# Kernel tuning notes

Measured on AMD Instinct MI355X. Metric: run time of the kernel, lower is better.

## Reference

```python
import jax, jax.numpy as jnp
import numpy as np

B, T, C = 2, 1024, 1024
H = 16
D = C // H          # 64 head_dim
NHH = 4             # hyper n_heads
NL = 2              # hyper n_layers
RANK = 8
SCALE = 16.0 / RANK # alpha / rank


def _rope(x, cos, sin):
    # x: (B,H,T,D); cos/sin: (1,1,T,D//2)
    xe, xo = x[..., ::2], x[..., 1::2]
    return jnp.stack((xe * cos - xo * sin, xe * sin + xo * cos), axis=-1).reshape(x.shape)


def _mha(x, w_in, b_in, w_out, b_out, mask):
    # torch nn.MultiheadAttention (batch_first) with additive causal mask
    b, t, d = x.shape
    dh = d // NHH
    qkv = x @ w_in.T + b_in
    q, k, v = jnp.split(qkv, 3, axis=-1)
    split = lambda z: z.reshape(b, t, NHH, dh).transpose(0, 2, 1, 3)
    q, k, v = split(q), split(k), split(v)
    s = jnp.einsum('bhqd,bhkd->bhqk', q, k) / jnp.sqrt(jnp.float32(dh)) + mask
    o = jnp.einsum('bhqk,bhkd->bhqd', jax.nn.softmax(s, axis=-1), v)
    o = o.transpose(0, 2, 1, 3).reshape(b, t, d)
    return o @ w_out.T + b_out


def _tiny_head(x_h, in_w, in_b, out_w, out_b, a_w, b_w, mask):
    # x_h: (B,T,D); per-layer params stacked on axis 0 (NL)
    out = x_h
    for l in range(NL):
        out = _mha(out, in_w[l], in_b[l], out_w[l], out_b[l], mask)
    ctx = out.mean(axis=1)                       # (B,D)
    A = (ctx @ a_w.T).reshape(-1, D, RANK)       # (B,D,R)
    Bm = (ctx @ b_w.T).reshape(-1, RANK, D)      # (B,R,D)
    return A, Bm


def reference(x, cos, sin, c_attn_w, c_attn_b, c_proj_w, c_proj_b,
              hyper_in_w, hyper_in_b, hyper_out_w, hyper_out_b, toA_w, toB_w):
    mask = jnp.where(jnp.tril(jnp.ones((T, T), bool)), 0.0, -jnp.inf).astype(x.dtype)
    qkv = x @ c_attn_w.T + c_attn_b
    q, k, v = jnp.split(qkv, 3, axis=-1)
    split = lambda z: z.reshape(B, T, H, D).transpose(0, 2, 1, 3)  # (B,H,T,D)
    q, k, v = split(q), split(k), split(v)
    q = _rope(q, cos, sin)
    k = _rope(k, cos, sin)
    x_heads = split(x)
    # vmap over the 16 main heads; each gets its own TinyHeadTransformer params
    A, Bm = jax.vmap(_tiny_head, in_axes=(1, 0, 0, 0, 0, 0, 0, None))(
        x_heads, hyper_in_w, hyper_in_b, hyper_out_w, hyper_out_b, toA_w, toB_w, mask)
    # A: (H,B,D,R), Bm: (H,B,R,D)
    delta_v = jnp.einsum('bhti,hbir,hbro->bhto', v, A, Bm)
    v = v + SCALE * delta_v
    s = jnp.einsum('bhqd,bhkd->bhqk', q, k) / jnp.sqrt(jnp.float32(D)) + mask
    y = jnp.einsum('bhqk,bhkd->bhqd', jax.nn.softmax(s, axis=-1), v)
    y = y.transpose(0, 2, 1, 3).reshape(B, T, C)
    return y @ c_proj_w.T + c_proj_b


def setup_inputs() -> dict:
    key = jax.random.key(0)
    ks = jax.random.split(key, 8)
    inv_freq = 1.0 / (10000.0 ** (jnp.arange(0, D, 2, dtype=jnp.float32) / D))
    ang = jnp.arange(T, dtype=jnp.float32)[:, None] * inv_freq[None, :]
    cos = jnp.cos(ang)[None, None]  # (1,1,T,D/2)
    sin = jnp.sin(ang)[None, None]
    g = lambda k, shape, sc: jax.random.normal(k, shape, jnp.float32) * sc
    return dict(
        x=g(ks[0], (B, T, C), 1.0),
        cos=cos, sin=sin,
        c_attn_w=g(ks[1], (3 * C, C), 0.02),
        c_attn_b=jnp.zeros((3 * C,), jnp.float32),
        c_proj_w=g(ks[2], (C, C), 0.02),
        c_proj_b=jnp.zeros((C,), jnp.float32),
        hyper_in_w=g(ks[3], (H, NL, 3 * D, D), 0.02),
        hyper_in_b=jnp.zeros((H, NL, 3 * D), jnp.float32),
        hyper_out_w=g(ks[4], (H, NL, D, D), 0.02),
        hyper_out_b=jnp.zeros((H, NL, D), jnp.float32),
        toA_w=g(ks[5], (H, D * RANK, D), 0.02),
        toB_w=g(ks[6], (H, RANK * D, D), 0.02),
    )
```

## Files before the change

### kernel.cpp

```cpp
#include <hip/hip_runtime.h>

typedef unsigned short u16;
typedef short v8s __attribute__((ext_vector_type(8)));
typedef short v4s16 __attribute__((ext_vector_type(4)));
typedef float v4f __attribute__((ext_vector_type(4)));

#if defined(__has_builtin)
#  if __has_builtin(__builtin_amdgcn_exp2f)
#    define EXP2F(x) __builtin_amdgcn_exp2f(x)
#  else
#    define EXP2F(x) exp2f(x)
#  endif
#else
#  define EXP2F(x) exp2f(x)
#endif

__device__ __forceinline__ float bf2f(u16 u){
  union { float f; unsigned int i; } c; c.i = ((unsigned int)u) << 16; return c.f;
}
__device__ __forceinline__ u16 f2bf(float f){
  union { float f; unsigned int i; } c; c.f = f;
  unsigned int r = c.i + 0x7FFFu + ((c.i >> 16) & 1u);
  return (u16)(r >> 16);
}
__device__ __forceinline__ unsigned int cvt_pk_bf16(float lo, float hi){
  unsigned int r;
  asm("v_cvt_pk_bf16_f32 %0, %1, %2" : "=v"(r) : "v"(lo), "v"(hi));
  return r;
}

struct CvtArgs {
  const float* s[13];
  u16* d[13];
  int n[13];
  int bstart[14];
  float* ctxz;
};
__global__ __launch_bounds__(256) void cvt_all(CvtArgs a) {
  if ((int)blockIdx.x >= a.bstart[13]) {
    float4 z = {0.f, 0.f, 0.f, 0.f};
    ((float4*)a.ctxz)[threadIdx.x] = z;
    ((float4*)a.ctxz)[256 + threadIdx.x] = z;
    return;
  }
  int j = 0;
  #pragma unroll
  for (int i = 1; i < 13; i++) if ((int)blockIdx.x >= a.bstart[i]) j = i;
  const int lb = blockIdx.x - a.bstart[j];
  const long base = (long)lb * 1024 + threadIdx.x * 4;
  if (base < a.n[j]) {
    const float4 f = *(const float4*)&a.s[j][base];
    v4s16 o;
    o.x = (short)f2bf(f.x); o.y = (short)f2bf(f.y);
    o.z = (short)f2bf(f.z); o.w = (short)f2bf(f.w);
    *(v4s16*)&a.d[j][base] = o;
  }
}

template<int BM, int BN, int EPI>
__global__ __launch_bounds__(256) void gemm_nt(
    const u16* __restrict__ A, long aBatch, int lda,
    const u16* __restrict__ W, long wBatch,
    const u16* __restrict__ bias, long bBatch,
    void* __restrict__ Cp, long cBatch, int ldc,
    int K,
    const u16* __restrict__ cosb, const u16* __restrict__ sinb,
    u16* __restrict__ q_r, u16* __restrict__ k_r, u16* __restrict__ v_out,
    float* __restrict__ ctxp)
{
  constexpr int BK = 64, LDT = BK + 8;
  constexpr int AC = BM / 32;
  constexpr int BC = BN / 32;
  A    += (long)blockIdx.z * aBatch;
  W    += (long)blockIdx.z * wBatch;
  bias += (long)blockIdx.z * bBatch;
  const int row0 = blockIdx.y * BM, col0 = blockIdx.x * BN;
  __shared__ __align__(16) u16 As[BM * LDT];
  __shared__ __align__(16) u16 Bs[BN * LDT];
  const int tid = threadIdx.x, wid = tid >> 6, lane = tid & 63;
  constexpr int FM = (BM/2)/16, FN = (BN/2)/16;
  const int wr = (wid >> 1) * (BM/2), wc = (wid & 1) * (BN/2);
  v4f acc[FM][FN] = {};
  const int lr = lane & 15, lk = (lane >> 4) * 8;

  v8s areg[AC], breg[BC];
  auto loadAB = [&](int k0) {
    #pragma unroll
    for (int i = 0; i < AC; i++) {
      const int c = tid + i*256, r = c >> 3, cc = (c & 7) * 8;
      areg[i] = *(const v8s*)&A[(long)(row0 + r)*lda + k0 + cc];
    }
    #pragma unroll
    for (int i = 0; i < BC; i++) {
      const int c = tid + i*256, r = c >> 3, cc = (c & 7) * 8;
      breg[i] = *(const v8s*)&W[(long)(col0 + r)*K + k0 + cc];
    }
  };
  auto writeAB = [&]() {
    #pragma unroll
    for (int i = 0; i < AC; i++) {
      const int c = tid + i*256, r = c >> 3, cc = (c & 7) * 8;
      *(v8s*)&As[r*LDT + cc] = areg[i];
    }
    #pragma unroll
    for (int i = 0; i < BC; i++) {
      const int c = tid + i*256, r = c >> 3, cc = (c & 7) * 8;
      *(v8s*)&Bs[r*LDT + cc] = breg[i];
    }
  };

  loadAB(0); writeAB();
  __syncthreads();
  for (int k0 = 0; k0 < K; k0 += BK) {
    if (k0 + BK < K) loadAB(k0 + BK);
    #pragma unroll
    for (int ks = 0; ks < BK; ks += 32) {
      v8s af[FM], bfv[FN];
      #pragma unroll
      for (int i = 0; i < FM; i++) af[i]  = *(const v8s*)&As[(wr + i*16 + lr)*LDT + ks + lk];
      #pragma unroll
      for (int j = 0; j < FN; j++) bfv[j] = *(const v8s*)&Bs[(wc + j*16 + lr)*LDT + ks + lk];
      #pragma unroll
      for (int i = 0; i < FM; i++)
        #pragma unroll
        for (int j = 0; j < FN; j++)
          acc[i][j] = __builtin_amdgcn_mfma_f32_16x16x32_bf16(af[i], bfv[j], acc[i][j], 0, 0, 0);
    }
    __syncthreads();
    if (k0 + BK < K) {
      writeAB();
      __syncthreads();
    }
  }
  const int lc = lane & 15, lq = (lane >> 4) * 4;
  if (EPI <= 1) {
    u16*   Cb = (u16*)Cp   + (long)blockIdx.z * cBatch;
    float* Cf = (float*)Cp + (long)blockIdx.z * cBatch;
    #pragma unroll
    for (int i = 0; i < FM; i++)
      #pragma unroll
      for (int j = 0; j < FN; j++) {
        const int cidx = col0 + wc + j*16 + lc;
        const float bv = bf2f(bias[cidx]);
        #pragma unroll
        for (int q = 0; q < 4; q++) {
          const int r = row0 + wr + i*16 + lq + q;
          if (EPI == 1) Cf[(long)r*ldc + cidx] = acc[i][j][q] + bv;
          else          Cb[(long)r*ldc + cidx] = f2bf(acc[i][j][q] + bv);
        }
      }
  } else if (EPI == 2) {
    #pragma unroll
    for (int i = 0; i < FM; i++)
      #pragma unroll
      for (int j = 0; j < FN; j++) {
        const int cidx = col0 + wc + j*16 + lc;
        const float bv = bf2f(bias[cidx]);
        const int which = cidx >> 10;
        const int h = (cidx & 1023) >> 6;
        const int d = cidx & 63;
        u16* dst = (which == 0) ? q_r : (which == 1) ? k_r : v_out;
        #pragma unroll
        for (int q = 0; q < 4; q++) {
          const int r = row0 + wr + i*16 + lq + q;
          const int b = r >> 10, t = r & 1023;
          float val = acc[i][j][q] + bv;
          float par = __shfl_xor(val, 1);
          float outv;
          if (which == 2) {
            outv = val;
          } else {
            const int i2 = d >> 1;
            const float cc = bf2f(cosb[(t << 5) + i2]);
            const float ss = bf2f(sinb[(t << 5) + i2]);
            outv = (d & 1) ? __builtin_fmaf(par, ss,  val*cc)
                           : __builtin_fmaf(val, cc, -par*ss);
          }
          dst[((long)((b << 4) + h)*1024 + t)*64 + d] = f2bf(outv);
        }
      }
  } else {
    const float inv = 1.0f/1024.0f;
    const int hb = (blockIdx.z << 1) + (row0 >> 10);
    #pragma unroll
    for (int j = 0; j < FN; j++) {
      const int cidx = col0 + wc + j*16 + lc;
      const float bv = bf2f(bias[cidx]);
      float p = (float)(FM*4) * bv;
      #pragma unroll
      for (int i = 0; i < FM; i++)
        #pragma unroll
        for (int q = 0; q < 4; q++) p += acc[i][j][q];
      p += __shfl_xor(p, 16);
      p += __shfl_xor(p, 32);
      if (lane < 16) atomicAdd(&ctxp[hb*64 + cidx], p * inv);
    }
  }
}

template<int D>
__global__ __launch_bounds__(512) void flash_mfma(
    const u16* __restrict__ qb, const u16* __restrict__ kb,
    const u16* __restrict__ vb, u16* __restrict__ ob,
    float scale, int n1, int n2,
    long q0, long q1, long q2, int qs,
    long k0, long k1, long k2, int ks,
    long v0, long v1, long v2, int vs,
    long o0, long o1, long o2, int os)
{
  constexpr int KBLK = 128;
  constexpr int NF  = KBLK / 16;
  constexpr int NKB = KBLK / 32;
  constexpr int KD2 = (D < 32) ? 32 : D;
  constexpr int LDK = KD2 + 8;
  constexpr int LDV = KBLK + 8;
  constexpr int KD  = KD2 / 32;
  constexpr int NSUB = D / 16;
  constexpr int KCH = KBLK * (KD2/8);
  constexpr int VCH = (D/8) * KBLK;
  constexpr int KIT = (KCH + 511) / 512;
  constexpr int VIT = (VCH + 511) / 512;
  __shared__ __align__(16) u16 Ks[2][KBLK * LDK];
  __shared__ __align__(16) u16 Vs[2][D * LDV];

  const int tid = threadIdx.x, wid = tid >> 6, lane = tid & 63;
  const int lr = lane & 15, lg = lane >> 4;
  const int prob = blockIdx.x;
  const int p2 = prob % n2, p1 = (prob / n2) % n1, p0 = prob / (n2 * n1);
  const u16* qp = qb + p0*q0 + p1*q1 + p2*q2;
  const u16* kp = kb + p0*k0 + p1*k1 + p2*k2;
  const u16* vp = vb + p0*v0 + p1*v1 + p2*v2;
  u16* op = ob + p0*o0 + p1*o1 + p2*o2;

  const int ta = blockIdx.y;
  const int tbt = 15 - ta;
  const int wtile = (wid & 4) ? tbt : ta;
  const int wq = wtile * 64 + (wid & 3) * 16;
  const int nchb = (tbt >> 1) + 1;
  const float scale2 = scale * 1.44269504f;

  v8s qf[KD];
  #pragma unroll
  for (int kd = 0; kd < KD; kd++) {
    const int dof = kd*32 + lg*8;
    v8s val = {};
    if (dof < D) val = *(const v8s*)&qp[(long)(wq + lr)*qs + dof];
    qf[kd] = val;
  }

  v4f Of[NSUB] = {};
  float m2 = -1.0e30f, l = 0.f;

  v8s kreg[KIT], vreg[VIT];
  auto loadK = [&](int kc) {
    #pragma unroll
    for (int i = 0; i < KIT; i++) {
      const int idx = tid + i*512;
      if (idx < KCH) {
        const int key = idx / (KD2/8), d8 = (idx % (KD2/8)) * 8;
        v8s t = {};
        if (d8 < D) t = *(const v8s*)&kp[(long)(kc + key)*ks + d8];
        kreg[i] = t;
      }
    }
  };
  auto loadV = [&](int kc) {
    #pragma unroll
    for (int i = 0; i < VIT; i++) {
      const int idx = tid + i*512;
      if (idx < VCH) {
        const int key = idx / (D/8), d8 = (idx % (D/8)) * 8;
        vreg[i] = *(const v8s*)&vp[(long)(kc + key)*vs + d8];
      }
    }
  };
  auto writeKV = [&](int buf) {
    #pragma unroll
    for (int i = 0; i < KIT; i++) {
      const int idx = tid + i*512;
      if (idx < KCH) {
        const int key = idx / (KD2/8), d8 = (idx % (KD2/8)) * 8;
        *(v8s*)&Ks[buf][key*LDK + d8] = kreg[i];
      }
    }
    #pragma unroll
    for (int i = 0; i < VIT; i++) {
      const int idx = tid + i*512;
      if (idx < VCH) {
        const int key = idx / (D/8), d8 = (idx % (D/8)) * 8;
        #pragma unroll
        for (int j = 0; j < 8; j++) Vs[buf][(d8+j)*LDV + key] = vreg[i][j];
      }
    }
  };

  loadK(0); loadV(0); writeKV(0);
  __syncthreads();

  for (int c = 0; c < nchb; c++) {
    const int cur = c & 1, nxt = cur ^ 1;
    if (c + 1 < nchb) { loadK((c+1)*KBLK); loadV((c+1)*KBLK); }
    const int kc = c * KBLK;
    if (kc <= wq + 15) {
      v4f sf[NF];
      #pragma unroll
      for (int f = 0; f < NF; f++) {
        v4f s = {};
        #pragma unroll
        for (int kd = 0; kd < KD; kd++) {
          const v8s kf = *(const v8s*)&Ks[cur][(f*16 + lr)*LDK + kd*32 + lg*8];
          s = __builtin_amdgcn_mfma_f32_16x16x32_bf16(kf, qf[kd], s, 0, 0, 0);
        }
        sf[f] = s;
      }
      const int qg = wq + lr;
      if (kc + KBLK - 1 > wq) {
        #pragma unroll
        for (int f = 0; f < NF; f++)
          #pragma unroll
          for (int r = 0; r < 4; r++)
            sf[f][r] = (kc + 16*f + 4*lg + r <= qg) ? sf[f][r] : -3.0e38f;
      }
      float mx = -3.0e38f;
      #pragma unroll
      for (int f = 0; f < NF; f++)
        mx = fmaxf(mx, fmaxf(fmaxf(sf[f][0], sf[f][1]), fmaxf(sf[f][2], sf[f][3])));
      mx = fmaxf(mx, __shfl_xor(mx, 16));
      mx = fmaxf(mx, __shfl_xor(mx, 32));
      const float mn2 = fmaxf(m2, mx * scale2);
      const float al = EXP2F(m2 - mn2);
      m2 = mn2;
      float pv[NF][4];
      float ps = 0.f;
      #pragma unroll
      for (int f = 0; f < NF; f++) {
        #pragma unroll
        for (int r = 0; r < 4; r++)
          pv[f][r] = EXP2F(__builtin_fmaf(sf[f][r], scale2, -mn2));
        ps += (pv[f][0] + pv[f][1]) + (pv[f][2] + pv[f][3]);
      }
      ps += __shfl_xor(ps, 16);
      ps += __shfl_xor(ps, 32);
      l = l * al + ps;
      #pragma unroll
      for (int sub = 0; sub < NSUB; sub++)
        #pragma unroll
        for (int r = 0; r < 4; r++) Of[sub][r] *= al;
      unsigned int pw[2*NF];
      #pragma unroll
      for (int f = 0; f < NF; f++) {
        pw[2*f]   = cvt_pk_bf16(pv[f][0], pv[f][1]);
        pw[2*f+1] = cvt_pk_bf16(pv[f][2], pv[f][3]);
      }
      #pragma unroll
      for (int kb2 = 0; kb2 < NKB; kb2++) {
        union { unsigned int w[4]; v8s v; } pb;
        pb.w[0] = pw[4*kb2];   pb.w[1] = pw[4*kb2+1];
        pb.w[2] = pw[4*kb2+2]; pb.w[3] = pw[4*kb2+3];
        #pragma unroll
        for (int sub = 0; sub < NSUB; sub++) {
          union { v4s16 h[2]; v8s v; } va;
          const int vbase = (sub*16 + lr)*LDV + kb2*32 + 4*lg;
          va.h[0] = *(const v4s16*)&Vs[cur][vbase];
          va.h[1] = *(const v4s16*)&Vs[cur][vbase + 16];
          Of[sub] = __builtin_amdgcn_mfma_f32_16x16x32_bf16(va.v, pb.v, Of[sub], 0, 0, 0);
        }
      }
    }
    if (c + 1 < nchb) writeKV(nxt);
    __syncthreads();
  }
  const float rl = __builtin_amdgcn_rcpf(l);
  #pragma unroll
  for (int sub = 0; sub < NSUB; sub++) {
    unsigned int w0 = cvt_pk_bf16(Of[sub][0]*rl, Of[sub][1]*rl);
    unsigned int w1 = cvt_pk_bf16(Of[sub][2]*rl, Of[sub][3]*rl);
    unsigned int* dst = (unsigned int*)&op[(long)(wq + lr)*os + sub*16 + 4*lg];
    dst[0] = w0; dst[1] = w1;
  }
}

__global__ __launch_bounds__(256) void ab_proj_k(const float* __restrict__ ctx,
    const u16* __restrict__ toA, const u16* __restrict__ toB,
    float* __restrict__ Am, float* __restrict__ Bm)
{
  const int hb = blockIdx.x; const int h = hb >> 1;
  const float* c = ctx + hb * 64;
  for (int n = threadIdx.x; n < 512; n += 256) {
    const u16* wa = toA + ((long)h*512 + n) * 64;
    const u16* wb = toB + ((long)h*512 + n) * 64;
    float sa = 0.f, sb = 0.f;
    for (int i = 0; i < 64; i++) { sa += c[i]*bf2f(wa[i]); sb += c[i]*bf2f(wb[i]); }
    Am[hb*512 + n] = sa;
    Bm[hb*512 + n] = sb;
  }
}

__global__ __launch_bounds__(256) void delta_v_k(
    u16* __restrict__ v, const float* __restrict__ Am, const float* __restrict__ Bm)
{
  const long idx = (long)blockIdx.x * blockDim.x + threadIdx.x;
  const int h = (int)((idx >> 10) & 15);
  const int b = (int)(idx >> 14);
  u16* row = v + idx * 64;
  const float* A = Am + (h*2 + b) * 512;
  const float* B = Bm + (h*2 + b) * 512;
  float tmp[8] = {};
  #pragma unroll 8
  for (int d = 0; d < 64; d++) {
    const float vd = bf2f(row[d]);
    #pragma unroll
    for (int r = 0; r < 8; r++) tmp[r] += vd * A[d*8 + r];
  }
  #pragma unroll 8
  for (int d = 0; d < 64; d++) {
    float s = 0.f;
    #pragma unroll
    for (int r = 0; r < 8; r++) s += tmp[r] * B[r*64 + d];
    row[d] = f2bf(bf2f(row[d]) + 2.0f * s);
  }
}

extern "C" void kernel_launch(void* const* d_in, const int* in_sizes, int n_in,
                              void* d_out, int out_size, void* d_ws, size_t ws_size,
                              hipStream_t stream) {
  (void)in_sizes; (void)n_in; (void)out_size; (void)ws_size;
  float* out = (float*)d_out;

  char* ws = (char*)d_ws;
  size_t off = 0;
  auto alloc = [&](size_t bytes){ void* p = ws + off; off += (bytes + 255) & ~(size_t)255; return p; };

  static const int ns[13] = {2097152, 32768, 32768, 3145728, 3072, 1048576, 1024,
                             393216, 6144, 131072, 2048, 524288, 524288};
  u16* bufs[13];
  for (int i = 0; i < 13; i++) bufs[i] = (u16*)alloc((size_t)ns[i] * 2);
  u16* xb    = bufs[0];
  u16* cosb  = bufs[1];
  u16* sinb  = bufs[2];
  u16* attnw = bufs[3];
  u16* attnb = bufs[4];
  u16* projw = bufs[5];
  u16* projb = bufs[6];
  u16* hinw  = bufs[7];
  u16* hinb  = bufs[8];
  u16* houtw = bufs[9];
  u16* houtb = bufs[10];
  u16* toAb  = bufs[11];
  u16* toBb  = bufs[12];

  u16* q_r  = (u16*)alloc(2097152ull*2);
  u16* k_r  = (u16*)alloc(2097152ull*2);
  u16* v    = (u16*)alloc(2097152ull*2);
  u16* tqkv = (u16*)alloc(6291456ull*2);
  u16* tatt = (u16*)alloc(2097152ull*2);
  u16* tb0  = (u16*)alloc(2097152ull*2);
  u16* yat  = (u16*)alloc(2097152ull*2);
  float* ctx  = (float*)alloc(2048*4);
  float* Amat = (float*)alloc(16384*4);
  float* Bmat = (float*)alloc(16384*4);

  CvtArgs ca;
  int bacc = 0;
  for (int i = 0; i < 13; i++) {
    ca.s[i] = (const float*)d_in[i];
    ca.d[i] = bufs[i];
    ca.n[i] = ns[i];
    ca.bstart[i] = bacc;
    bacc += (ns[i] + 1023) / 1024;
  }
  ca.bstart[13] = bacc;
  ca.ctxz = ctx;
  cvt_all<<<dim3(bacc + 1), 256, 0, stream>>>(ca);

  gemm_nt<64,64,2><<<dim3(48,32,1),256,0,stream>>>(xb,0,1024, attnw,0, attnb,0,
      nullptr,0,0, 1024, cosb, sinb, q_r, k_r, v, nullptr);

  gemm_nt<64,64,0><<<dim3(3,32,16),256,0,stream>>>(xb, 64L, 1024,
      hinw, (long)2*192*64, hinb, (long)2*192,
      tqkv, (long)2048*192, 192, 64,
      nullptr, nullptr, nullptr, nullptr, nullptr, nullptr);
  flash_mfma<16><<<dim3(128,8),512,0,stream>>>(tqkv, tqkv+64, tqkv+128, tatt,
      0.25f, 2, 4,
      (long)2048*192, (long)1024*192, 16L, 192,
      (long)2048*192, (long)1024*192, 16L, 192,
      (long)2048*192, (long)1024*192, 16L, 192,
      (long)2048*64,  (long)1024*64,  16L, 64);
  gemm_nt<64,64,0><<<dim3(1,32,16),256,0,stream>>>(tatt, (long)2048*64, 64,
      houtw, (long)2*64*64, houtb, (long)2*64,
      tb0, (long)2048*64, 64, 64,
      nullptr, nullptr, nullptr, nullptr, nullptr, nullptr);
  gemm_nt<64,64,0><<<dim3(3,32,16),256,0,stream>>>(tb0, (long)2048*64, 64,
      hinw + (size_t)192*64, (long)2*192*64, hinb + 192, (long)2*192,
      tqkv, (long)2048*192, 192, 64,
      nullptr, nullptr, nullptr, nullptr, nullptr, nullptr);
  flash_mfma<16><<<dim3(128,8),512,0,stream>>>(tqkv, tqkv+64, tqkv+128, tatt,
      0.25f, 2, 4,
      (long)2048*192, (long)1024*192, 16L, 192,
      (long)2048*192, (long)1024*192, 16L, 192,
      (long)2048*192, (long)1024*192, 16L, 192,
      (long)2048*64,  (long)1024*64,  16L, 64);
  gemm_nt<64,64,3><<<dim3(1,32,16),256,0,stream>>>(tatt, (long)2048*64, 64,
      houtw + (size_t)64*64, (long)2*64*64, houtb + 64, (long)2*64,
      nullptr, 0, 0, 64,
      nullptr, nullptr, nullptr, nullptr, nullptr, ctx);

  ab_proj_k<<<dim3(32),256,0,stream>>>(ctx, toAb, toBb, Amat, Bmat);
  delta_v_k<<<dim3(128),256,0,stream>>>(v, Amat, Bmat);

  flash_mfma<64><<<dim3(32,8),512,0,stream>>>(q_r, k_r, v, yat,
      0.125f, 16, 1,
      (long)16*1024*64, (long)1024*64, 0L, 64,
      (long)16*1024*64, (long)1024*64, 0L, 64,
      (long)16*1024*64, (long)1024*64, 0L, 64,
      (long)1024*1024,  64L,           0L, 1024);

  gemm_nt<64,64,1><<<dim3(16,32,1),256,0,stream>>>(yat,0,1024, projw,0, projb,0,
      out,0,1024, 1024,
      nullptr, nullptr, nullptr, nullptr, nullptr, nullptr);
}
```

Before: 274.8 us.

## Fold layer-0 out-proj into layer-1 in-proj, double-buffer GEMM smem, fuse AB/delta

```diff
diff --git a/kernel.cpp b/kernel.cpp
--- a/kernel.cpp
+++ b/kernel.cpp
@@ -54,6 +54,38 @@
     o.x = (short)f2bf(f.x); o.y = (short)f2bf(f.y);
     o.z = (short)f2bf(f.z); o.w = (short)f2bf(f.w);
     *(v4s16*)&a.d[j][base] = o;
+  }
+}
+
+__global__ __launch_bounds__(256) void wcomb_k(
+    const u16* __restrict__ hinw, const u16* __restrict__ hinb,
+    const u16* __restrict__ houtw, const u16* __restrict__ houtb,
+    u16* __restrict__ wcomb, u16* __restrict__ bcomb)
+{
+  const int h = blockIdx.x, tid = threadIdx.x;
+  const u16* win1  = hinw  + ((size_t)h*2 + 1) * 192*64;
+  const u16* bin1  = hinb  + ((size_t)h*2 + 1) * 192;
+  const u16* wout0 = houtw + (size_t)h*2 * 64*64;
+  const u16* bout0 = houtb + (size_t)h*2 * 64;
+  __shared__ float wo[64][64];
+  __shared__ float bo[64];
+  for (int i = tid; i < 4096; i += 256) wo[i >> 6][i & 63] = bf2f(wout0[i]);
+  if (tid < 64) bo[tid] = bf2f(bout0[tid]);
+  __syncthreads();
+  for (int idx = tid; idx < 12288; idx += 256) {
+    const int n = idx >> 6, i = idx & 63;
+    const u16* wr = win1 + n*64;
+    float s = 0.f;
+    #pragma unroll 8
+    for (int o = 0; o < 64; o++) s += bf2f(wr[o]) * wo[o][i];
+    wcomb[((size_t)h*192 + n)*64 + i] = f2bf(s);
+  }
+  if (tid < 192) {
+    const u16* wr = win1 + tid*64;
+    float s = bf2f(bin1[tid]);
+    #pragma unroll 8
+    for (int o = 0; o < 64; o++) s += bf2f(wr[o]) * bo[o];
+    bcomb[(size_t)h*192 + tid] = f2bf(s);
   }
 }
 
@@ -75,8 +107,8 @@
   W    += (long)blockIdx.z * wBatch;
   bias += (long)blockIdx.z * bBatch;
   const int row0 = blockIdx.y * BM, col0 = blockIdx.x * BN;
-  __shared__ __align__(16) u16 As[BM * LDT];
-  __shared__ __align__(16) u16 Bs[BN * LDT];
+  __shared__ __align__(16) u16 As[2][BM * LDT];
+  __shared__ __align__(16) u16 Bs[2][BN * LDT];
   const int tid = threadIdx.x, wid = tid >> 6, lane = tid & 63;
   constexpr int FM = (BM/2)/16, FN = (BN/2)/16;
   const int wr = (wid >> 1) * (BM/2), wc = (wid & 1) * (BN/2);
@@ -96,41 +128,40 @@
       breg[i] = *(const v8s*)&W[(long)(col0 + r)*K + k0 + cc];
     }
   };
-  auto writeAB = [&]() {
+  auto writeAB = [&](int buf) {
     #pragma unroll
     for (int i = 0; i < AC; i++) {
       const int c = tid + i*256, r = c >> 3, cc = (c & 7) * 8;
-      *(v8s*)&As[r*LDT + cc] = areg[i];
+      *(v8s*)&As[buf][r*LDT + cc] = areg[i];
     }
     #pragma unroll
     for (int i = 0; i < BC; i++) {
       const int c = tid + i*256, r = c >> 3, cc = (c & 7) * 8;
-      *(v8s*)&Bs[r*LDT + cc] = breg[i];
+      *(v8s*)&Bs[buf][r*LDT + cc] = breg[i];
     }
   };
 
-  loadAB(0); writeAB();
+  loadAB(0); writeAB(0);
   __syncthreads();
-  for (int k0 = 0; k0 < K; k0 += BK) {
-    if (k0 + BK < K) loadAB(k0 + BK);
+  const int NIT = K / BK;
+  for (int it = 0; it < NIT; it++) {
+    const int cur = it & 1;
+    if (it + 1 < NIT) loadAB((it + 1) * BK);
     #pragma unroll
     for (int ks = 0; ks < BK; ks += 32) {
       v8s af[FM], bfv[FN];
       #pragma unroll
-      for (int i = 0; i < FM; i++) af[i]  = *(const v8s*)&As[(wr + i*16 + lr)*LDT + ks + lk];
-      #pragma unroll
-      for (int j = 0; j < FN; j++) bfv[j] = *(const v8s*)&Bs[(wc + j*16 + lr)*LDT + ks + lk];
+      for (int i = 0; i < FM; i++) af[i]  = *(const v8s*)&As[cur][(wr + i*16 + lr)*LDT + ks + lk];
+      #pragma unroll
+      for (int j = 0; j < FN; j++) bfv[j] = *(const v8s*)&Bs[cur][(wc + j*16 + lr)*LDT + ks + lk];
       #pragma unroll
       for (int i = 0; i < FM; i++)
         #pragma unroll
         for (int j = 0; j < FN; j++)
           acc[i][j] = __builtin_amdgcn_mfma_f32_16x16x32_bf16(af[i], bfv[j], acc[i][j], 0, 0, 0);
     }
+    if (it + 1 < NIT) writeAB(cur ^ 1);
     __syncthreads();
-    if (k0 + BK < K) {
-      writeAB();
-      __syncthreads();
-    }
   }
   const int lc = lane & 15, lq = (lane >> 4) * 4;
   if (EPI <= 1) {
@@ -380,44 +411,44 @@
   }
 }
 
-__global__ __launch_bounds__(256) void ab_proj_k(const float* __restrict__ ctx,
+__global__ __launch_bounds__(256) void abdelta_k(const float* __restrict__ ctx,
     const u16* __restrict__ toA, const u16* __restrict__ toB,
-    float* __restrict__ Am, float* __restrict__ Bm)
+    u16* __restrict__ v)
 {
-  const int hb = blockIdx.x; const int h = hb >> 1;
-  const float* c = ctx + hb * 64;
-  for (int n = threadIdx.x; n < 512; n += 256) {
+  const int hb = blockIdx.x;
+  const int h = hb >> 1, b = hb & 1;
+  const int tid = threadIdx.x;
+  __shared__ float Am[512];
+  __shared__ float Bm[512];
+  __shared__ float cf[64];
+  if (tid < 64) cf[tid] = ctx[hb*64 + tid];
+  __syncthreads();
+  for (int n = tid; n < 512; n += 256) {
     const u16* wa = toA + ((long)h*512 + n) * 64;
     const u16* wb = toB + ((long)h*512 + n) * 64;
     float sa = 0.f, sb = 0.f;
-    for (int i = 0; i < 64; i++) { sa += c[i]*bf2f(wa[i]); sb += c[i]*bf2f(wb[i]); }
-    Am[hb*512 + n] = sa;
-    Bm[hb*512 + n] = sb;
-  }
-}
-
-__global__ __launch_bounds__(256) void delta_v_k(
-    u16* __restrict__ v, const float* __restrict__ Am, const float* __restrict__ Bm)
-{
-  const long idx = (long)blockIdx.x * blockDim.x + threadIdx.x;
-  const int h = (int)((idx >> 10) & 15);
-  const int b = (int)(idx >> 14);
-  u16* row = v + idx * 64;
-  const float* A = Am + (h*2 + b) * 512;
-  const float* B = Bm + (h*2 + b) * 512;
-  float tmp[8] = {};
-  #pragma unroll 8
-  for (int d = 0; d < 64; d++) {
-    const float vd = bf2f(row[d]);
-    #pragma unroll
-    for (int r = 0; r < 8; r++) tmp[r] += vd * A[d*8 + r];
-  }
-  #pragma unroll 8
-  for (int d = 0; d < 64; d++) {
-    float s = 0.f;
-    #pragma unroll
-    for (int r = 0; r < 8; r++) s += tmp[r] * B[r*64 + d];
-    row[d] = f2bf(bf2f(row[d]) + 2.0f * s);
+    #pragma unroll 8
+    for (int i = 0; i < 64; i++) { sa += cf[i]*bf2f(wa[i]); sb += cf[i]*bf2f(wb[i]); }
+    Am[n] = sa; Bm[n] = sb;
+  }
+  __syncthreads();
+  u16* base = v + ((long)(b*16 + h)*1024)*64;
+  for (int t = tid; t < 1024; t += 256) {
+    u16* row = base + (long)t*64;
+    float tmp[8] = {};
+    #pragma unroll 8
+    for (int d = 0; d < 64; d++) {
+      const float vd = bf2f(row[d]);
+      #pragma unroll
+      for (int r = 0; r < 8; r++) tmp[r] += vd * Am[d*8 + r];
+    }
+    #pragma unroll 8
+    for (int d = 0; d < 64; d++) {
+      float s = 0.f;
+      #pragma unroll
+      for (int r = 0; r < 8; r++) s += tmp[r] * Bm[r*64 + d];
+      row[d] = f2bf(bf2f(row[d]) + 2.0f * s);
+    }
   }
 }
 
@@ -449,16 +480,15 @@
   u16* toAb  = bufs[11];
   u16* toBb  = bufs[12];
 
-  u16* q_r  = (u16*)alloc(2097152ull*2);
-  u16* k_r  = (u16*)alloc(2097152ull*2);
-  u16* v    = (u16*)alloc(2097152ull*2);
-  u16* tqkv = (u16*)alloc(6291456ull*2);
-  u16* tatt = (u16*)alloc(2097152ull*2);
-  u16* tb0  = (u16*)alloc(2097152ull*2);
-  u16* yat  = (u16*)alloc(2097152ull*2);
+  u16* q_r   = (u16*)alloc(2097152ull*2);
+  u16* k_r   = (u16*)alloc(2097152ull*2);
+  u16* v     = (u16*)alloc(2097152ull*2);
+  u16* tqkv  = (u16*)alloc(6291456ull*2);
+  u16* tatt  = (u16*)alloc(2097152ull*2);
+  u16* yat   = (u16*)alloc(2097152ull*2);
+  u16* wcomb = (u16*)alloc(196608ull*2);
+  u16* bcomb = (u16*)alloc(3072ull*2);
   float* ctx  = (float*)alloc(2048*4);
-  float* Amat = (float*)alloc(16384*4);
-  float* Bmat = (float*)alloc(16384*4);
 
   CvtArgs ca;
   int bacc = 0;
@@ -472,6 +502,8 @@
   ca.bstart[13] = bacc;
   ca.ctxz = ctx;
   cvt_all<<<dim3(bacc + 1), 256, 0, stream>>>(ca);
+
+  wcomb_k<<<dim3(16), 256, 0, stream>>>(hinw, hinb, houtw, houtb, wcomb, bcomb);
 
   gemm_nt<64,64,2><<<dim3(48,32,1),256,0,stream>>>(xb,0,1024, attnw,0, attnb,0,
       nullptr,0,0, 1024, cosb, sinb, q_r, k_r, v, nullptr);
@@ -486,12 +518,8 @@
       (long)2048*192, (long)1024*192, 16L, 192,
       (long)2048*192, (long)1024*192, 16L, 192,
       (long)2048*64,  (long)1024*64,  16L, 64);
-  gemm_nt<64,64,0><<<dim3(1,32,16),256,0,stream>>>(tatt, (long)2048*64, 64,
-      houtw, (long)2*64*64, houtb, (long)2*64,
-      tb0, (long)2048*64, 64, 64,
-      nullptr, nullptr, nullptr, nullptr, nullptr, nullptr);
-  gemm_nt<64,64,0><<<dim3(3,32,16),256,0,stream>>>(tb0, (long)2048*64, 64,
-      hinw + (size_t)192*64, (long)2*192*64, hinb + 192, (long)2*192,
+  gemm_nt<64,64,0><<<dim3(3,32,16),256,0,stream>>>(tatt, (long)2048*64, 64,
+      wcomb, (long)192*64, bcomb, 192L,
       tqkv, (long)2048*192, 192, 64,
       nullptr, nullptr, nullptr, nullptr, nullptr, nullptr);
   flash_mfma<16><<<dim3(128,8),512,0,stream>>>(tqkv, tqkv+64, tqkv+128, tatt,
@@ -505,8 +533,7 @@
       nullptr, 0, 0, 64,
       nullptr, nullptr, nullptr, nullptr, nullptr, ctx);
 
-  ab_proj_k<<<dim3(32),256,0,stream>>>(ctx, toAb, toBb, Amat, Bmat);
-  delta_v_k<<<dim3(128),256,0,stream>>>(v, Amat, Bmat);
+  abdelta_k<<<dim3(32),256,0,stream>>>(ctx, toAb, toBb, v);
 
   flash_mfma<64><<<dim3(32,8),512,0,stream>>>(q_r, k_r, v, yat,
       0.125f, 16, 1,
```

After: 327.8 us. 1.19x slower.
